# Kernel optimization log

Measured on AMD Instinct MI355X. Metric: run time of the kernel, lower is better.

## Reference

```python
import jax, jax.numpy as jnp
import numpy as np

N_RES = 4096
N_PAIRS = 500000

def setup_inputs() -> dict:
    key = jax.random.key(0)
    k1, k2, k3 = jax.random.split(key, 3)
    ca_coords = jax.random.normal(k1, (N_RES, 3), dtype=jnp.float32) * 10.0
    K = jax.random.uniform(k2, (N_RES, N_RES), dtype=jnp.float32)
    pairs = jax.random.randint(k3, (N_PAIRS, 2), 0, N_RES, dtype=jnp.int64)
    return {"ca_coords": ca_coords, "K": K, "pairs": pairs}


def _reconstruct_backbone(ca):
    # vectorized version of reconstruct_backbone_atoms
    n = ca.shape[0]
    vec = ca[1:] - ca[:-1]                                  # (n-1,3)
    unit = vec / (jnp.linalg.norm(vec, axis=-1, keepdims=True) + 1e-8)
    # N atoms: n_coords[i] = ca[i] - 0.38*unit(ca[i]-ca[i-1]); n_coords[0] uses unit[0]
    n_coords = jnp.concatenate([ca[:1] - 0.38 * unit[:1], ca[1:] - 0.38 * unit], axis=0)
    # C atoms: c_coords[i] = ca[i] + 0.38*unit(ca[i+1]-ca[i]); c_coords[-1] uses unit[-1]
    c_coords = jnp.concatenate([ca[:-1] + 0.38 * unit, ca[-1:] + 0.38 * unit[-1:]], axis=0)
    # O atoms: perpendicular to (C-CA, N-CA) plane, last residue special-cased
    vec_n = n_coords[:-1] - ca[:-1]
    vec_c = c_coords[:-1] - ca[:-1]
    perp = jnp.cross(vec_c, vec_n)
    pnorm = jnp.linalg.norm(perp, axis=-1, keepdims=True)
    perp = jnp.where(pnorm > 1e-6, perp / jnp.maximum(pnorm, 1e-12), perp)
    o_body = c_coords[:-1] + 1.24 * perp
    o_last = c_coords[-1:] + jnp.array([[0.0, 1.24, 0.0]], dtype=ca.dtype)
    o_coords = jnp.concatenate([o_body, o_last], axis=0)
    return n_coords, c_coords, o_coords


def _pairwise_dist(x, y):
    # safe cdist: sqrt clamped so diagonal zeros stay differentiable
    sq = jnp.sum((x[:, None, :] - y[None, :, :]) ** 2, axis=-1)
    return jnp.sqrt(jnp.maximum(sq, 1e-12))


def reference(ca_coords, K, pairs):
    n = ca_coords.shape[0]

    # --- bond energy (weight=30): mean((|ca[i+1]-ca[i]| - 3.8)^2) ---
    d_bond = jnp.linalg.norm(ca_coords[1:] - ca_coords[:-1], axis=-1)
    e_bond = 30.0 * jnp.mean((d_bond - 3.8) ** 2)

    # --- clash energy (weight=50): mean(relu(3.2 - d_pair)^2) ---
    dv = ca_coords[pairs[:, 0]] - ca_coords[pairs[:, 1]]
    d_pair = jnp.sqrt(jnp.maximum(jnp.sum(dv ** 2, axis=-1), 1e-12))
    e_clash = 50.0 * jnp.mean(jax.nn.relu(3.2 - d_pair) ** 2)

    # --- contact energy (weight=5): mean((D - 8*(1-K))^2) over full NxN ---
    D = _pairwise_dist(ca_coords, ca_coords)
    target = 8.0 * (1.0 - K)
    e_contact = 5.0 * jnp.mean((D - target) ** 2)

    # --- hydrogen bond energy (weight=4) from reconstructed backbone ---
    n_coords, c_coords, o_coords = _reconstruct_backbone(ca_coords)
    ideal = 2.95
    hb = jnp.float32(0.0)
    # double loop i, j in [i+2, i+6) -> offsets 2..5, vectorized per offset
    for off in (2, 3, 4, 5):
        d = jnp.linalg.norm(o_coords[: n - off] - n_coords[off:], axis=-1)
        pen = jnp.exp(-(((d - ideal) / 0.3) ** 2))
        hb = hb - 0.5 * jnp.sum(jnp.where((d > 2.5) & (d < 3.5), pen, 0.0))
    e_hb = 4.0 * hb / (n * n)

    return e_bond + e_clash + e_contact + e_hb
```

## Files before the change

kernel.cpp:

```cpp
#include <hip/hip_runtime.h>
#include <math.h>

#define NRES 4096
#define CONTACT_ROWS 8
#define CONTACT_BLOCKS 512
#define CLASH_BLOCKS   256
#define BOND_BLOCKS    16

__device__ __forceinline__ void block_reduce_atomic(float v, float* red, float* dst) {
#pragma unroll
    for (int off = 32; off > 0; off >>= 1) v += __shfl_down(v, off, 64);
    if ((threadIdx.x & 63) == 0) red[threadIdx.x >> 6] = v;
    __syncthreads();
    if (threadIdx.x == 0) atomicAdd(dst, red[0] + red[1] + red[2] + red[3]);
    __syncthreads();
}

__global__ __launch_bounds__(256) void energy_kernel(const float* __restrict__ ca,
                                                     const float* __restrict__ K,
                                                     const int* __restrict__ pairs,
                                                     float* __restrict__ acc,
                                                     int n, int npairs) {
    __shared__ float sx[NRES], sy[NRES], sz[NRES];
    __shared__ float red[4];
    int tid = threadIdx.x;
    for (int j = tid; j < n; j += 256) {
        sx[j] = ca[3*j+0];
        sy[j] = ca[3*j+1];
        sz[j] = ca[3*j+2];
    }
    __syncthreads();

    int b = blockIdx.x;

    if (b < CONTACT_BLOCKS) {
        int row0 = b * CONTACT_ROWS;
        float lsum = 0.f;
        int nq = n >> 2;
#pragma unroll
        for (int r = 0; r < CONTACT_ROWS; ++r) {
            int i = row0 + r;
            float xi = sx[i], yi = sy[i], zi = sz[i];
            const float4* Krow4 = (const float4*)(K + (size_t)i * n);
            for (int j4 = tid; j4 < nq; j4 += 256) {
                float4 kv = Krow4[j4];
                int j = j4 << 2;
                float4 cx = *(const float4*)&sx[j];
                float4 cy = *(const float4*)&sy[j];
                float4 cz = *(const float4*)&sz[j];

                float dx, dy, dz, sq, D, t;
                dx = xi - cx.x; dy = yi - cy.x; dz = zi - cz.x;
                sq = dx*dx + dy*dy + dz*dz;
                D  = sqrtf(fmaxf(sq, 1e-12f));
                t  = D - 8.0f*(1.0f - kv.x);  lsum += t*t;

                dx = xi - cx.y; dy = yi - cy.y; dz = zi - cz.y;
                sq = dx*dx + dy*dy + dz*dz;
                D  = sqrtf(fmaxf(sq, 1e-12f));
                t  = D - 8.0f*(1.0f - kv.y);  lsum += t*t;

                dx = xi - cx.z; dy = yi - cy.z; dz = zi - cz.z;
                sq = dx*dx + dy*dy + dz*dz;
                D  = sqrtf(fmaxf(sq, 1e-12f));
                t  = D - 8.0f*(1.0f - kv.z);  lsum += t*t;

                dx = xi - cx.w; dy = yi - cy.w; dz = zi - cz.w;
                sq = dx*dx + dy*dy + dz*dz;
                D  = sqrtf(fmaxf(sq, 1e-12f));
                t  = D - 8.0f*(1.0f - kv.w);  lsum += t*t;
            }
        }
        block_reduce_atomic(lsum, red, acc + 2);

    } else if (b < CONTACT_BLOCKS + CLASH_BLOCKS) {
        int cb = b - CONTACT_BLOCKS;
        float v = 0.f;
        for (int p = cb * 256 + tid; p < npairs; p += CLASH_BLOCKS * 256) {
            int i0 = pairs[2*p + 0];
            int i1 = pairs[2*p + 1];
            float dx = sx[i0] - sx[i1];
            float dy = sy[i0] - sy[i1];
            float dz = sz[i0] - sz[i1];
            float d  = sqrtf(fmaxf(dx*dx + dy*dy + dz*dz, 1e-12f));
            float r  = fmaxf(3.2f - d, 0.f);
            v += r * r;
        }
        block_reduce_atomic(v, red, acc + 1);

    } else {
        int ib = b - CONTACT_BLOCKS - CLASH_BLOCKS;
        int i = ib * 256 + tid;
        float bond = 0.f, hb = 0.f;

        if (i < n - 1) {
            float dx = sx[i+1] - sx[i];
            float dy = sy[i+1] - sy[i];
            float dz = sz[i+1] - sz[i];
            float d  = sqrtf(dx*dx + dy*dy + dz*dz);
            float t  = d - 3.8f;
            bond = t * t;
        }

        if (i < n - 2) {
            float cax = sx[i], cay = sy[i], caz = sz[i];
            float vx = sx[i+1] - cax, vy = sy[i+1] - cay, vz = sz[i+1] - caz;
            float inv = 1.f / (sqrtf(vx*vx + vy*vy + vz*vz) + 1e-8f);
            float ux = vx*inv, uy = vy*inv, uz = vz*inv;

            float upx, upy, upz;
            if (i == 0) { upx = ux; upy = uy; upz = uz; }
            else {
                float wx = cax - sx[i-1], wy = cay - sy[i-1], wz = caz - sz[i-1];
                float inv2 = 1.f / (sqrtf(wx*wx + wy*wy + wz*wz) + 1e-8f);
                upx = wx*inv2; upy = wy*inv2; upz = wz*inv2;
            }

            float vcx = 0.38f*ux,  vcy = 0.38f*uy,  vcz = 0.38f*uz;
            float vnx = -0.38f*upx, vny = -0.38f*upy, vnz = -0.38f*upz;
            float px = vcy*vnz - vcz*vny;
            float py = vcz*vnx - vcx*vnz;
            float pz = vcx*vny - vcy*vnx;
            float pn = sqrtf(px*px + py*py + pz*pz);
            if (pn > 1e-6f) {
                float ipn = 1.f / fmaxf(pn, 1e-12f);
                px *= ipn; py *= ipn; pz *= ipn;
            }
            float ox = cax + vcx + 1.24f*px;
            float oy = cay + vcy + 1.24f*py;
            float oz = caz + vcz + 1.24f*pz;

#pragma unroll
            for (int off = 2; off <= 5; ++off) {
                int j = i + off;
                if (j < n) {
                    float cjx = sx[j], cjy = sy[j], cjz = sz[j];
                    float qx = cjx - sx[j-1], qy = cjy - sy[j-1], qz = cjz - sz[j-1];
                    float invq = 1.f / (sqrtf(qx*qx + qy*qy + qz*qz) + 1e-8f);
                    float njx = cjx - 0.38f*qx*invq;
                    float njy = cjy - 0.38f*qy*invq;
                    float njz = cjz - 0.38f*qz*invq;
                    float ddx = ox - njx, ddy = oy - njy, ddz = oz - njz;
                    float d = sqrtf(ddx*ddx + ddy*ddy + ddz*ddz);
                    if (d > 2.5f && d < 3.5f) {
                        float z = (d - 2.95f) * (1.0f / 0.3f);
                        hb -= 0.5f * expf(-z*z);
                    }
                }
            }
        }

        block_reduce_atomic(bond, red, acc + 0);
        block_reduce_atomic(hb,   red, acc + 3);
    }
}

__global__ void finalize_kernel(const float* __restrict__ acc, float* __restrict__ out,
                                int n, int npairs) {
    float e_bond    = 30.f * acc[0] / (float)(n - 1);
    float e_clash   = 50.f * acc[1] / (float)npairs;
    float inv_nn    = 1.f / ((float)n * (float)n);
    float e_contact = 5.f * acc[2] * inv_nn;
    float e_hb      = 4.f * acc[3] * inv_nn;
    out[0] = e_bond + e_clash + e_contact + e_hb;
}

extern "C" void kernel_launch(void* const* d_in, const int* in_sizes, int n_in,
                              void* d_out, int out_size, void* d_ws, size_t ws_size,
                              hipStream_t stream) {
    const float* ca    = (const float*)d_in[0];
    const float* K     = (const float*)d_in[1];
    const int*   pairs = (const int*)d_in[2];
    float* out = (float*)d_out;
    float* acc = (float*)d_ws;

    int n      = in_sizes[0] / 3;
    int npairs = in_sizes[2] / 2;

    hipMemsetAsync(acc, 0, 4 * sizeof(float), stream);

    int grid = CONTACT_BLOCKS + CLASH_BLOCKS + BOND_BLOCKS;
    energy_kernel<<<grid, 256, 0, stream>>>(ca, K, pairs, acc, n, npairs);
    finalize_kernel<<<1, 1, 0, stream>>>(acc, out, n, npairs);
}
```

Before: 116.4 us.

## Merge all energy terms into uniform blocks with per-block partials and no atomics

Every one of 512 blocks now computes its 8 contact rows, a strided share of the clash pairs, and the bond/hbond terms for its 8 residues. The contact loop is restructured to load 8 K rows per column chunk and reuse the shared coordinates across rows. Per-block partial sums are written to workspace and reduced by a 256-thread finalize kernel, which removes the memset and the global atomics. Each block now carries mixed work, so load balance relies on the clash loop being cheap, and register pressure rises from holding 8 float4 K values.

```diff
diff --git a/kernel.cpp b/kernel.cpp
--- a/kernel.cpp
+++ b/kernel.cpp
@@ -1,117 +1,116 @@
 #include <hip/hip_runtime.h>
 #include <math.h>
 
-#define NRES 4096
-#define CONTACT_ROWS 8
-#define CONTACT_BLOCKS 512
-#define CLASH_BLOCKS   256
-#define BOND_BLOCKS    16
-
-__device__ __forceinline__ void block_reduce_atomic(float v, float* red, float* dst) {
+#define NRES   4096
+#define NBLK   512
+#define ROWS   8
+#define NQ     (NRES / 4)
+#define CHUNKS (NQ / 256)
+
+__device__ __forceinline__ float wave_sum(float v) {
 #pragma unroll
     for (int off = 32; off > 0; off >>= 1) v += __shfl_down(v, off, 64);
-    if ((threadIdx.x & 63) == 0) red[threadIdx.x >> 6] = v;
-    __syncthreads();
-    if (threadIdx.x == 0) atomicAdd(dst, red[0] + red[1] + red[2] + red[3]);
-    __syncthreads();
+    return v;
 }
 
 __global__ __launch_bounds__(256) void energy_kernel(const float* __restrict__ ca,
                                                      const float* __restrict__ K,
                                                      const int* __restrict__ pairs,
-                                                     float* __restrict__ acc,
-                                                     int n, int npairs) {
+                                                     float4* __restrict__ partial,
+                                                     int npairs) {
     __shared__ float sx[NRES], sy[NRES], sz[NRES];
-    __shared__ float red[4];
-    int tid = threadIdx.x;
-    for (int j = tid; j < n; j += 256) {
+    __shared__ float red[4][4];
+    const int tid = threadIdx.x;
+    const int b   = blockIdx.x;
+
+    for (int j = tid; j < NRES; j += 256) {
         sx[j] = ca[3*j+0];
         sy[j] = ca[3*j+1];
         sz[j] = ca[3*j+2];
     }
     __syncthreads();
 
-    int b = blockIdx.x;
-
-    if (b < CONTACT_BLOCKS) {
-        int row0 = b * CONTACT_ROWS;
-        float lsum = 0.f;
-        int nq = n >> 2;
-#pragma unroll
-        for (int r = 0; r < CONTACT_ROWS; ++r) {
-            int i = row0 + r;
-            float xi = sx[i], yi = sy[i], zi = sz[i];
-            const float4* Krow4 = (const float4*)(K + (size_t)i * n);
-            for (int j4 = tid; j4 < nq; j4 += 256) {
-                float4 kv = Krow4[j4];
-                int j = j4 << 2;
-                float4 cx = *(const float4*)&sx[j];
-                float4 cy = *(const float4*)&sy[j];
-                float4 cz = *(const float4*)&sz[j];
-
-                float dx, dy, dz, sq, D, t;
-                dx = xi - cx.x; dy = yi - cy.x; dz = zi - cz.x;
-                sq = dx*dx + dy*dy + dz*dz;
-                D  = sqrtf(fmaxf(sq, 1e-12f));
-                t  = D - 8.0f*(1.0f - kv.x);  lsum += t*t;
-
-                dx = xi - cx.y; dy = yi - cy.y; dz = zi - cz.y;
-                sq = dx*dx + dy*dy + dz*dz;
-                D  = sqrtf(fmaxf(sq, 1e-12f));
-                t  = D - 8.0f*(1.0f - kv.y);  lsum += t*t;
-
-                dx = xi - cx.z; dy = yi - cy.z; dz = zi - cz.z;
-                sq = dx*dx + dy*dy + dz*dz;
-                D  = sqrtf(fmaxf(sq, 1e-12f));
-                t  = D - 8.0f*(1.0f - kv.z);  lsum += t*t;
-
-                dx = xi - cx.w; dy = yi - cy.w; dz = zi - cz.w;
-                sq = dx*dx + dy*dy + dz*dz;
-                D  = sqrtf(fmaxf(sq, 1e-12f));
-                t  = D - 8.0f*(1.0f - kv.w);  lsum += t*t;
-            }
+    const int row0 = b * ROWS;
+    float xi[ROWS], yi[ROWS], zi[ROWS];
+#pragma unroll
+    for (int r = 0; r < ROWS; ++r) {
+        xi[r] = sx[row0 + r]; yi[r] = sy[row0 + r]; zi[r] = sz[row0 + r];
+    }
+
+    float contact = 0.f;
+    const float4* Kp = (const float4*)(K + (size_t)row0 * NRES);
+#pragma unroll
+    for (int k = 0; k < CHUNKS; ++k) {
+        const int j4 = tid + (k << 8);
+        float4 kv[ROWS];
+#pragma unroll
+        for (int r = 0; r < ROWS; ++r) kv[r] = Kp[(size_t)r * NQ + j4];
+        const int j = j4 << 2;
+        const float4 cx = *(const float4*)&sx[j];
+        const float4 cy = *(const float4*)&sy[j];
+        const float4 cz = *(const float4*)&sz[j];
+#pragma unroll
+        for (int r = 0; r < ROWS; ++r) {
+            float dx, dy, dz, sq, D, t;
+            dx = xi[r]-cx.x; dy = yi[r]-cy.x; dz = zi[r]-cz.x;
+            sq = fmaf(dx, dx, fmaf(dy, dy, dz*dz));
+            D  = sqrtf(fmaxf(sq, 1e-12f));
+            t  = fmaf(8.f, kv[r].x, D - 8.f);
+            contact = fmaf(t, t, contact);
+
+            dx = xi[r]-cx.y; dy = yi[r]-cy.y; dz = zi[r]-cz.y;
+            sq = fmaf(dx, dx, fmaf(dy, dy, dz*dz));
+            D  = sqrtf(fmaxf(sq, 1e-12f));
+            t  = fmaf(8.f, kv[r].y, D - 8.f);
+            contact = fmaf(t, t, contact);
+
+            dx = xi[r]-cx.z; dy = yi[r]-cy.z; dz = zi[r]-cz.z;
+            sq = fmaf(dx, dx, fmaf(dy, dy, dz*dz));
+            D  = sqrtf(fmaxf(sq, 1e-12f));
+            t  = fmaf(8.f, kv[r].z, D - 8.f);
+            contact = fmaf(t, t, contact);
+
+            dx = xi[r]-cx.w; dy = yi[r]-cy.w; dz = zi[r]-cz.w;
+            sq = fmaf(dx, dx, fmaf(dy, dy, dz*dz));
+            D  = sqrtf(fmaxf(sq, 1e-12f));
+            t  = fmaf(8.f, kv[r].w, D - 8.f);
+            contact = fmaf(t, t, contact);
         }
-        block_reduce_atomic(lsum, red, acc + 2);
-
-    } else if (b < CONTACT_BLOCKS + CLASH_BLOCKS) {
-        int cb = b - CONTACT_BLOCKS;
-        float v = 0.f;
-        for (int p = cb * 256 + tid; p < npairs; p += CLASH_BLOCKS * 256) {
-            int i0 = pairs[2*p + 0];
-            int i1 = pairs[2*p + 1];
-            float dx = sx[i0] - sx[i1];
-            float dy = sy[i0] - sy[i1];
-            float dz = sz[i0] - sz[i1];
-            float d  = sqrtf(fmaxf(dx*dx + dy*dy + dz*dz, 1e-12f));
-            float r  = fmaxf(3.2f - d, 0.f);
-            v += r * r;
-        }
-        block_reduce_atomic(v, red, acc + 1);
-
-    } else {
-        int ib = b - CONTACT_BLOCKS - CLASH_BLOCKS;
-        int i = ib * 256 + tid;
-        float bond = 0.f, hb = 0.f;
+    }
+
+    float clash = 0.f;
+    for (int p = b * 256 + tid; p < npairs; p += NBLK * 256) {
+        int2 pr = ((const int2*)pairs)[p];
+        float dx = sx[pr.x] - sx[pr.y];
+        float dy = sy[pr.x] - sy[pr.y];
+        float dz = sz[pr.x] - sz[pr.y];
+        float d  = sqrtf(fmaxf(fmaf(dx, dx, fmaf(dy, dy, dz*dz)), 1e-12f));
+        float r  = fmaxf(3.2f - d, 0.f);
+        clash = fmaf(r, r, clash);
+    }
+
+    float bond = 0.f, hb = 0.f;
+    if (tid < ROWS) {
+        const int i = row0 + tid;
+        const int n = NRES;
 
         if (i < n - 1) {
-            float dx = sx[i+1] - sx[i];
-            float dy = sy[i+1] - sy[i];
-            float dz = sz[i+1] - sz[i];
-            float d  = sqrtf(dx*dx + dy*dy + dz*dz);
+            float dx = sx[i+1]-sx[i], dy = sy[i+1]-sy[i], dz = sz[i+1]-sz[i];
+            float d  = sqrtf(fmaf(dx, dx, fmaf(dy, dy, dz*dz)));
             float t  = d - 3.8f;
             bond = t * t;
         }
 
         if (i < n - 2) {
             float cax = sx[i], cay = sy[i], caz = sz[i];
-            float vx = sx[i+1] - cax, vy = sy[i+1] - cay, vz = sz[i+1] - caz;
+            float vx = sx[i+1]-cax, vy = sy[i+1]-cay, vz = sz[i+1]-caz;
             float inv = 1.f / (sqrtf(vx*vx + vy*vy + vz*vz) + 1e-8f);
             float ux = vx*inv, uy = vy*inv, uz = vz*inv;
 
             float upx, upy, upz;
             if (i == 0) { upx = ux; upy = uy; upz = uz; }
             else {
-                float wx = cax - sx[i-1], wy = cay - sy[i-1], wz = caz - sz[i-1];
+                float wx = cax-sx[i-1], wy = cay-sy[i-1], wz = caz-sz[i-1];
                 float inv2 = 1.f / (sqrtf(wx*wx + wy*wy + wz*wz) + 1e-8f);
                 upx = wx*inv2; upy = wy*inv2; upz = wz*inv2;
             }
@@ -132,15 +131,15 @@
 
 #pragma unroll
             for (int off = 2; off <= 5; ++off) {
-                int j = i + off;
-                if (j < n) {
-                    float cjx = sx[j], cjy = sy[j], cjz = sz[j];
-                    float qx = cjx - sx[j-1], qy = cjy - sy[j-1], qz = cjz - sz[j-1];
+                int jj = i + off;
+                if (jj < n) {
+                    float cjx = sx[jj], cjy = sy[jj], cjz = sz[jj];
+                    float qx = cjx-sx[jj-1], qy = cjy-sy[jj-1], qz = cjz-sz[jj-1];
                     float invq = 1.f / (sqrtf(qx*qx + qy*qy + qz*qz) + 1e-8f);
                     float njx = cjx - 0.38f*qx*invq;
                     float njy = cjy - 0.38f*qy*invq;
                     float njz = cjz - 0.38f*qz*invq;
-                    float ddx = ox - njx, ddy = oy - njy, ddz = oz - njz;
+                    float ddx = ox-njx, ddy = oy-njy, ddz = oz-njz;
                     float d = sqrtf(ddx*ddx + ddy*ddy + ddz*ddz);
                     if (d > 2.5f && d < 3.5f) {
                         float z = (d - 2.95f) * (1.0f / 0.3f);
@@ -149,20 +148,53 @@
                 }
             }
         }
-
-        block_reduce_atomic(bond, red, acc + 0);
-        block_reduce_atomic(hb,   red, acc + 3);
-    }
-}
-
-__global__ void finalize_kernel(const float* __restrict__ acc, float* __restrict__ out,
-                                int n, int npairs) {
-    float e_bond    = 30.f * acc[0] / (float)(n - 1);
-    float e_clash   = 50.f * acc[1] / (float)npairs;
-    float inv_nn    = 1.f / ((float)n * (float)n);
-    float e_contact = 5.f * acc[2] * inv_nn;
-    float e_hb      = 4.f * acc[3] * inv_nn;
-    out[0] = e_bond + e_clash + e_contact + e_hb;
+    }
+
+    float vb = wave_sum(bond);
+    float vc = wave_sum(clash);
+    float vk = wave_sum(contact);
+    float vh = wave_sum(hb);
+    const int wave = tid >> 6;
+    if ((tid & 63) == 0) {
+        red[wave][0] = vb; red[wave][1] = vc; red[wave][2] = vk; red[wave][3] = vh;
+    }
+    __syncthreads();
+    if (tid == 0) {
+        float4 out;
+        out.x = red[0][0] + red[1][0] + red[2][0] + red[3][0];
+        out.y = red[0][1] + red[1][1] + red[2][1] + red[3][1];
+        out.z = red[0][2] + red[1][2] + red[2][2] + red[3][2];
+        out.w = red[0][3] + red[1][3] + red[2][3] + red[3][3];
+        partial[b] = out;
+    }
+}
+
+__global__ __launch_bounds__(256) void finalize_kernel(const float4* __restrict__ partial,
+                                                       float* __restrict__ out,
+                                                       int n, int npairs) {
+    __shared__ float red[4][4];
+    const int tid = threadIdx.x;
+    float4 a = partial[tid];
+    float4 c = partial[tid + 256];
+    float vb = a.x + c.x, vc = a.y + c.y, vk = a.z + c.z, vh = a.w + c.w;
+    vb = wave_sum(vb); vc = wave_sum(vc); vk = wave_sum(vk); vh = wave_sum(vh);
+    const int wave = tid >> 6;
+    if ((tid & 63) == 0) {
+        red[wave][0] = vb; red[wave][1] = vc; red[wave][2] = vk; red[wave][3] = vh;
+    }
+    __syncthreads();
+    if (tid == 0) {
+        float bond    = red[0][0] + red[1][0] + red[2][0] + red[3][0];
+        float clash   = red[0][1] + red[1][1] + red[2][1] + red[3][1];
+        float contact = red[0][2] + red[1][2] + red[2][2] + red[3][2];
+        float hb      = red[0][3] + red[1][3] + red[2][3] + red[3][3];
+        float inv_nn  = 1.f / ((float)n * (float)n);
+        float e = 30.f * bond / (float)(n - 1)
+                + 50.f * clash / (float)npairs
+                + 5.f  * contact * inv_nn
+                + 4.f  * hb * inv_nn;
+        out[0] = e;
+    }
 }
 
 extern "C" void kernel_launch(void* const* d_in, const int* in_sizes, int n_in,
@@ -172,14 +204,11 @@
     const float* K     = (const float*)d_in[1];
     const int*   pairs = (const int*)d_in[2];
     float* out = (float*)d_out;
-    float* acc = (float*)d_ws;
+    float4* partial = (float4*)d_ws;
 
     int n      = in_sizes[0] / 3;
     int npairs = in_sizes[2] / 2;
 
-    hipMemsetAsync(acc, 0, 4 * sizeof(float), stream);
-
-    int grid = CONTACT_BLOCKS + CLASH_BLOCKS + BOND_BLOCKS;
-    energy_kernel<<<grid, 256, 0, stream>>>(ca, K, pairs, acc, n, npairs);
-    finalize_kernel<<<1, 1, 0, stream>>>(acc, out, n, npairs);
-}
+    energy_kernel<<<NBLK, 256, 0, stream>>>(ca, K, pairs, partial, npairs);
+    finalize_kernel<<<1, 256, 0, stream>>>(partial, out, n, npairs);
+}
```

Result: faster. 111.1 us (-4.6%).
